# Kernel tuning notes

Hardware: AMD Instinct MI355X
Metric: run time of the kernel (lower is better)

## Reference

```python
import jax, jax.numpy as jnp
import numpy as np

N_NODES = 10000
IN_DIM = 256
HIDDEN = 512
OUT_DIM = 256
N_EDGES = 320000


def setup_inputs() -> dict:
    key = jax.random.key(0)
    k1, k2, k3, k4, k5, k6 = jax.random.split(key, 6)
    x = jax.random.normal(k1, (N_NODES, IN_DIM), dtype=jnp.float32)
    edge_index = jax.random.randint(k2, (2, N_EDGES), 0, N_NODES, dtype=jnp.int64)
    s1 = 1.0 / np.sqrt(2 * IN_DIM)
    s2 = 1.0 / np.sqrt(HIDDEN)
    W1 = jax.random.uniform(k3, (2 * IN_DIM, HIDDEN), jnp.float32, -s1, s1)
    b1 = jax.random.uniform(k4, (HIDDEN,), jnp.float32, -s1, s1)
    W2 = jax.random.uniform(k5, (HIDDEN, OUT_DIM), jnp.float32, -s2, s2)
    b2 = jax.random.uniform(k6, (OUT_DIM,), jnp.float32, -s2, s2)
    return {"x": x, "edge_index": edge_index, "W1": W1, "b1": b1, "W2": W2, "b2": b2}


def reference(x, edge_index, W1, b1, W2, b2):
    # x: [N, d]; edge_index: [2, E]
    x = x.reshape(-1, x.shape[-1])
    start, end = edge_index.reshape(2, -1)
    # gather + concat -> [E, 2d]
    ef = jnp.concatenate([x[start], x[end]], axis=1)
    h = jax.nn.relu(ef @ W1 + b1)          # [E, hidden]
    out = h @ W2 + b2                        # [E, out]
    return out.reshape(-1, edge_index.shape[1], out.shape[-1])  # [1, E, out]
```

## Files before the change

### kernel.cpp

```cpp
#include <hip/hip_runtime.h>
#include <cstdint>

#define E_TOTAL 320000
#define NN 10000
#define DIN 256
#define HDIM 512
#define DOUT 256
#define M_TILE 48
#define N_MAIN_BLOCKS ((E_TOTAL + M_TILE - 1) / M_TILE)

typedef __attribute__((ext_vector_type(8))) short short8;
typedef __attribute__((ext_vector_type(8))) unsigned short ushort8;
typedef __attribute__((ext_vector_type(4))) float f32x4;

__device__ __forceinline__ unsigned short f2bf(float f) {
    union { float f; unsigned u; } v; v.f = f;
    unsigned u = v.u;
    return (unsigned short)((u + 0x7fffu + ((u >> 16) & 1u)) >> 16);
}
__device__ __forceinline__ float bf2f(unsigned short u) {
    union { unsigned u; float f; } v; v.u = ((unsigned)u) << 16; return v.f;
}

__global__ void detect_i64(const int* __restrict__ eidx, int* __restrict__ flag) {
    __shared__ int anynz;
    if (threadIdx.x == 0) anynz = 0;
    __syncthreads();
    int v = 0;
    for (int i = threadIdx.x; i < 8192; i += blockDim.x) v |= eidx[2 * i + 1];
    if (v != 0) atomicOr(&anynz, 1);
    __syncthreads();
    if (threadIdx.x == 0) *flag = (anynz == 0) ? 1 : 0;
}

__global__ void convert_x(const float* __restrict__ x, unsigned short* __restrict__ xb) {
    int total = NN * DIN;
    for (int i = blockIdx.x * blockDim.x + threadIdx.x; i < total; i += gridDim.x * blockDim.x)
        xb[i] = f2bf(x[i]);
}

__global__ void pack_w(const float* __restrict__ W, unsigned short* __restrict__ Wp,
                       int ncols, int nct, int nks) {
    int tid = blockIdx.x * blockDim.x + threadIdx.x;
    int total = nct * nks * 64;
    if (tid >= total) return;
    int lane = tid & 63;
    int ks = (tid >> 6) % nks;
    int ct = tid / (64 * nks);
    int k0 = ks * 32 + (lane >> 4) * 8;
    int n = ct * 16 + (lane & 15);
    short8 v;
#pragma unroll
    for (int j = 0; j < 8; j++) v[j] = (short)f2bf(W[(long)(k0 + j) * ncols + n]);
    *(short8*)(Wp + ((long)(ct * nks + ks) * 64 + lane) * 8) = v;
}

__global__ void pack_wcat(const float* __restrict__ W1, unsigned short* __restrict__ Wp) {
    int tid = blockIdx.x * blockDim.x + threadIdx.x;
    if (tid >= 64 * 8 * 64) return;
    int lane = tid & 63;
    int ks = (tid >> 6) & 7;
    int ct = tid >> 9;
    int k0 = ks * 32 + (lane >> 4) * 8;
    int n = ct * 16 + (lane & 15);
    int col = n & 511;
    int radd = (n >> 9) * 256;
    short8 v;
#pragma unroll
    for (int j = 0; j < 8; j++) v[j] = (short)f2bf(W1[(long)(k0 + j + radd) * HDIM + col]);
    *(short8*)(Wp + ((long)(ct * 8 + ks) * 64 + lane) * 8) = v;
}

template<bool PF32>
__global__ __launch_bounds__(256, 2)
void node_gemm(const unsigned short* __restrict__ xb,
               const unsigned short* __restrict__ Wcp,
               void* __restrict__ Pv)
{
    __shared__ unsigned short xs[64 * 256];
    const int tid = threadIdx.x;
    const int lane = tid & 63;
    const int w = tid >> 6;
    const int lo = lane & 15;
    const int quad = lane >> 4;
    const int rt0 = blockIdx.x;
    const int cq = blockIdx.y;

#pragma unroll
    for (int i = 0; i < 8; i++) {
        int rp = i * 4 + w;
        int r = rp * 2 + (lane >> 5);
        int node = rt0 * 64 + r;
        if (node > NN - 1) node = NN - 1;
        int cs = (lane & 31) ^ (r & 7);
        const unsigned short* g = xb + (long)node * DIN + cs * 8;
        unsigned roff = __builtin_amdgcn_readfirstlane((unsigned)(rp * 512));
        __builtin_amdgcn_global_load_lds(
            (const __attribute__((address_space(1))) void*)g,
            (__attribute__((address_space(3))) void*)(xs + roff),
            16, 0, 0);
    }
    __syncthreads();

    f32x4 acc[4][4];
#pragma unroll
    for (int rt = 0; rt < 4; rt++)
#pragma unroll
        for (int ct = 0; ct < 4; ct++) acc[rt][ct] = (f32x4){0.f, 0.f, 0.f, 0.f};

    short8 ap[2][4], bp[2][4];
    auto loadA = [&](short8* d, int ks) {
#pragma unroll
        for (int rt = 0; rt < 4; rt++) {
            int m = rt * 16 + lo;
            int c = (ks * 4 + quad) ^ (m & 7);
            d[rt] = *(const short8*)(xs + m * 256 + c * 8);
        }
    };
    auto loadB = [&](short8* d, int ks) {
#pragma unroll
        for (int ct = 0; ct < 4; ct++) {
            int ctg = cq * 16 + w * 4 + ct;
            d[ct] = *(const short8*)(Wcp + ((long)(ctg * 8 + ks) * 64 + lane) * 8);
        }
    };
    loadA(ap[0], 0);
    loadB(bp[0], 0);
#pragma unroll
    for (int ks = 0; ks < 8; ks++) {
        int cur = ks & 1, nxt = cur ^ 1;
        if (ks < 7) { loadA(ap[nxt], ks + 1); loadB(bp[nxt], ks + 1); }
#pragma unroll
        for (int ct = 0; ct < 4; ct++)
#pragma unroll
            for (int rt = 0; rt < 4; rt++)
                acc[rt][ct] = __builtin_amdgcn_mfma_f32_16x16x32_bf16(
                    ap[cur][rt], bp[cur][ct], acc[rt][ct], 0, 0, 0);
    }

#pragma unroll
    for (int rt = 0; rt < 4; rt++) {
#pragma unroll
        for (int rr = 0; rr < 4; rr++) {
            int r = rt0 * 64 + rt * 16 + quad * 4 + rr;
            if (r < NN) {
                long off = (long)r * 1024 + cq * 256 + w * 64 + lo;
#pragma unroll
                for (int ct = 0; ct < 4; ct++) {
                    float v = acc[rt][ct][rr];
                    if constexpr (PF32) ((float*)Pv)[off + ct * 16] = v;
                    else ((unsigned short*)Pv)[off + ct * 16] = f2bf(v);
                }
            }
        }
    }
}

template<bool PF32>
__global__ __launch_bounds__(512, 4)
void edge_out(const void* __restrict__ Pv,
              const int* __restrict__ eidx,
              const float* __restrict__ b1,
              const unsigned short* __restrict__ W2p,
              const float* __restrict__ b2,
              const int* __restrict__ flag,
              float* __restrict__ out)
{
    __shared__ unsigned short hs[64 * 512];
    const int tid = threadIdx.x;
    const int lane = tid & 63;
    const int w = tid >> 6;
    const int lo = lane & 15;
    const int quad = lane >> 4;
    const long e0 = (long)blockIdx.x * 64;

    const bool is64 = (*flag != 0);
    int snv, tnv;
    {
        long e = e0 + w * 8 + (lane & 7);
        long s, t;
        if (is64) {
            s = ((const long long*)eidx)[e];
            t = ((const long long*)eidx)[E_TOTAL + e];
        } else {
            s = eidx[e];
            t = eidx[E_TOTAL + e];
        }
        if (s < 0) s = 0; if (s > NN - 1) s = NN - 1;
        if (t < 0) t = 0; if (t > NN - 1) t = NN - 1;
        snv = (int)s; tnv = (int)t;
    }
    f32x4 bia0 = *(const f32x4*)(b1 + lane * 8);
    f32x4 bia1 = *(const f32x4*)(b1 + lane * 8 + 4);

#pragma unroll
    for (int j = 0; j < 8; j++) {
        int sv = __shfl(snv, j, 8);
        int tv = __shfl(tnv, j, 8);
        int r = w * 8 + j;
        short8 hv;
        if constexpr (PF32) {
            const float* Ar = (const float*)Pv + (long)sv * 1024 + lane * 8;
            const float* Br = (const float*)Pv + (long)tv * 1024 + 512 + lane * 8;
            f32x4 a0 = *(const f32x4*)(Ar);
            f32x4 a1 = *(const f32x4*)(Ar + 4);
            f32x4 c0 = *(const f32x4*)(Br);
            f32x4 c1 = *(const f32x4*)(Br + 4);
#pragma unroll
            for (int jj = 0; jj < 4; jj++) {
                hv[jj]     = (short)f2bf(fmaxf(a0[jj] + c0[jj] + bia0[jj], 0.f));
                hv[jj + 4] = (short)f2bf(fmaxf(a1[jj] + c1[jj] + bia1[jj], 0.f));
            }
        } else {
            const unsigned short* Ar = (const unsigned short*)Pv + (long)sv * 1024 + lane * 8;
            const unsigned short* Br = (const unsigned short*)Pv + (long)tv * 1024 + 512 + lane * 8;
            ushort8 av = *(const ushort8*)(Ar);
            ushort8 cv = *(const ushort8*)(Br);
#pragma unroll
            for (int jj = 0; jj < 4; jj++) {
                hv[jj]     = (short)f2bf(fmaxf(bf2f(av[jj]) + bf2f(cv[jj]) + bia0[jj], 0.f));
                hv[jj + 4] = (short)f2bf(fmaxf(bf2f(av[jj + 4]) + bf2f(cv[jj + 4]) + bia1[jj], 0.f));
            }
        }
        *(short8*)(hs + r * 512 + ((lane ^ (r & 7)) << 3)) = hv;
    }
    __syncthreads();

    f32x4 oacc[4][2];
#pragma unroll
    for (int rt = 0; rt < 4; rt++)
#pragma unroll
        for (int ct = 0; ct < 2; ct++) oacc[rt][ct] = (f32x4){0.f, 0.f, 0.f, 0.f};

    short8 ap[2][4], bp[2][2];
    auto loadA2 = [&](short8* d, int ks) {
#pragma unroll
        for (int rt = 0; rt < 4; rt++) {
            int m = rt * 16 + lo;
            int c = (ks * 4 + quad) ^ (m & 7);
            d[rt] = *(const short8*)(hs + m * 512 + c * 8);
        }
    };
    auto loadB2 = [&](short8* d, int ks) {
#pragma unroll
        for (int ct = 0; ct < 2; ct++) {
            int ctg = w * 2 + ct;
            d[ct] = *(const short8*)(W2p + ((long)(ctg * 16 + ks) * 64 + lane) * 8);
        }
    };
    loadA2(ap[0], 0);
    loadB2(bp[0], 0);
#pragma unroll
    for (int ks = 0; ks < 16; ks++) {
        int cur = ks & 1, nxt = cur ^ 1;
        if (ks < 15) { loadA2(ap[nxt], ks + 1); loadB2(bp[nxt], ks + 1); }
#pragma unroll
        for (int ct = 0; ct < 2; ct++)
#pragma unroll
            for (int rt = 0; rt < 4; rt++)
                oacc[rt][ct] = __builtin_amdgcn_mfma_f32_16x16x32_bf16(
                    ap[cur][rt], bp[cur][ct], oacc[rt][ct], 0, 0, 0);
    }

    float bv[2];
#pragma unroll
    for (int ct = 0; ct < 2; ct++) bv[ct] = b2[w * 32 + ct * 16 + lo];
#pragma unroll
    for (int rt = 0; rt < 4; rt++) {
#pragma unroll
        for (int rr = 0; rr < 4; rr++) {
            int rwo = rt * 16 + quad * 4 + rr;
            float* op = out + (e0 + rwo) * DOUT + w * 32 + lo;
#pragma unroll
            for (int ct = 0; ct < 2; ct++)
                op[ct * 16] = oacc[rt][ct][rr] + bv[ct];
        }
    }
}

__global__ __launch_bounds__(256, 2)
void edge_mlp(const unsigned short* __restrict__ xb,
              const int* __restrict__ eidx,
              const float* __restrict__ b1,
              const unsigned short* __restrict__ W1p,
              const float* __restrict__ b2v_g,
              const unsigned short* __restrict__ W2p,
              const int* __restrict__ flag,
              float* __restrict__ out)
{
    __shared__ unsigned short ef[M_TILE * 512];
    __shared__ unsigned short hb[M_TILE * 128];

    const int tid = threadIdx.x;
    const int lane = tid & 63;
    const int w = tid >> 6;
    const int lo = lane & 15;
    const int quad = lane >> 4;
    const long e0 = (long)blockIdx.x * M_TILE;
    const bool is64 = (*flag != 0);

#pragma unroll
    for (int i = 0; i < 12; i++) {
        int r = i * 4 + w;
        long e = e0 + r;
        long ec = (e < E_TOTAL) ? e : 0;
        long sn, tn;
        if (is64) {
            sn = ((const long long*)eidx)[ec];
            tn = ((const long long*)eidx)[E_TOTAL + ec];
        } else {
            sn = eidx[ec];
            tn = eidx[E_TOTAL + ec];
        }
        long node = (lane < 32) ? sn : tn;
        int cih = (lane & 31) ^ (r & 7);
        const unsigned short* g = xb + node * DIN + cih * 8;
        unsigned roff = __builtin_amdgcn_readfirstlane((unsigned)(r * 512));
        __builtin_amdgcn_global_load_lds(
            (const __attribute__((address_space(1))) void*)g,
            (__attribute__((address_space(3))) void*)(ef + roff),
            16, 0, 0);
    }
    __syncthreads();

    f32x4 oacc[3][4];
#pragma unroll
    for (int rt = 0; rt < 3; rt++)
#pragma unroll
        for (int ct = 0; ct < 4; ct++)
            oacc[rt][ct] = (f32x4){0.f, 0.f, 0.f, 0.f};

    auto loadA1 = [&](short8* dst, int ks) {
#pragma unroll
        for (int rt = 0; rt < 3; rt++) {
            int m = rt * 16 + lo;
            int c = (ks * 4 + quad) ^ (m & 7);
            dst[rt] = *(const short8*)(ef + m * 512 + c * 8);
        }
    };

    for (int kc = 0; kc < 4; kc++) {
        short8 w2f[16];
#pragma unroll
        for (int s = 0; s < 4; s++)
#pragma unroll
            for (int ct = 0; ct < 4; ct++) {
                int ctg = w * 4 + ct;
                int ks2 = kc * 4 + s;
                w2f[s * 4 + ct] =
                    *(const short8*)(W2p + ((long)(ctg * 16 + ks2) * 64 + lane) * 8);
            }
        float b1v[2];
#pragma unroll
        for (int ct = 0; ct < 2; ct++) b1v[ct] = b1[kc * 128 + w * 32 + ct * 16 + lo];

        f32x4 hacc[3][2];
#pragma unroll
        for (int rt = 0; rt < 3; rt++)
#pragma unroll
            for (int ct = 0; ct < 2; ct++)
                hacc[rt][ct] = (f32x4){0.f, 0.f, 0.f, 0.f};

        short8 a_p[2][3], b_p[2][2];
        loadA1(a_p[0], 0);
#pragma unroll
        for (int ct = 0; ct < 2; ct++) {
            int ctg = kc * 8 + w * 2 + ct;
            b_p[0][ct] = *(const short8*)(W1p + ((long)(ctg * 16 + 0) * 64 + lane) * 8);
        }

#pragma unroll
        for (int ks = 0; ks < 16; ks++) {
            int cur = ks & 1, nxt = cur ^ 1;
            if (ks < 15) {
                loadA1(a_p[nxt], ks + 1);
#pragma unroll
                for (int ct = 0; ct < 2; ct++) {
                    int ctg = kc * 8 + w * 2 + ct;
                    b_p[nxt][ct] =
                        *(const short8*)(W1p + ((long)(ctg * 16 + ks + 1) * 64 + lane) * 8);
                }
            }
#pragma unroll
            for (int ct = 0; ct < 2; ct++)
#pragma unroll
                for (int rt = 0; rt < 3; rt++)
                    hacc[rt][ct] = __builtin_amdgcn_mfma_f32_16x16x32_bf16(
                        a_p[cur][rt], b_p[cur][ct], hacc[rt][ct], 0, 0, 0);
        }

#pragma unroll
        for (int ct = 0; ct < 2; ct++) {
            int cwl = w * 32 + ct * 16 + lo;
            float bias = b1v[ct];
            int c = cwl >> 3;
            int cb = cwl & 7;
#pragma unroll
            for (int rt = 0; rt < 3; rt++) {
#pragma unroll
                for (int rr = 0; rr < 4; rr++) {
                    int rw = rt * 16 + quad * 4 + rr;
                    float v = fmaxf(hacc[rt][ct][rr] + bias, 0.f);
                    hb[rw * 128 + ((c ^ (rw & 7)) << 3) + cb] = f2bf(v);
                }
            }
        }
        __syncthreads();

        short8 a2_p[2][3];
#pragma unroll
        for (int rt = 0; rt < 3; rt++) {
            int m = rt * 16 + lo;
            int c = (0 + quad) ^ (m & 7);
            a2_p[0][rt] = *(const short8*)(hb + m * 128 + c * 8);
        }
#pragma unroll
        for (int s = 0; s < 4; s++) {
            int cur = s & 1, nxt = cur ^ 1;
            if (s < 3) {
#pragma unroll
                for (int rt = 0; rt < 3; rt++) {
                    int m = rt * 16 + lo;
                    int c = ((s + 1) * 4 + quad) ^ (m & 7);
                    a2_p[nxt][rt] = *(const short8*)(hb + m * 128 + c * 8);
                }
            }
#pragma unroll
            for (int ct = 0; ct < 4; ct++)
#pragma unroll
                for (int rt = 0; rt < 3; rt++)
                    oacc[rt][ct] = __builtin_amdgcn_mfma_f32_16x16x32_bf16(
                        a2_p[cur][rt], w2f[s * 4 + ct], oacc[rt][ct], 0, 0, 0);
        }
        if (kc < 3) __syncthreads();
    }

    float bv[4];
#pragma unroll
    for (int ct = 0; ct < 4; ct++) bv[ct] = b2v_g[w * 64 + ct * 16 + lo];
#pragma unroll
    for (int rt = 0; rt < 3; rt++) {
#pragma unroll
        for (int rr = 0; rr < 4; rr++) {
            int rw = rt * 16 + quad * 4 + rr;
            long e = e0 + rw;
            if (e < E_TOTAL) {
                float* op = out + e * DOUT + w * 64 + lo;
#pragma unroll
                for (int ct = 0; ct < 4; ct++)
                    op[ct * 16] = oacc[rt][ct][rr] + bv[ct];
            }
        }
    }
}

extern "C" void kernel_launch(void* const* d_in, const int* in_sizes, int n_in,
                              void* d_out, int out_size, void* d_ws, size_t ws_size,
                              hipStream_t stream) {
    const float* x   = (const float*)d_in[0];
    const int*   ei  = (const int*)d_in[1];
    const float* W1  = (const float*)d_in[2];
    const float* b1  = (const float*)d_in[3];
    const float* W2  = (const float*)d_in[4];
    const float* b2  = (const float*)d_in[5];
    float* out = (float*)d_out;

    unsigned short* xb  = (unsigned short*)d_ws;
    unsigned short* Wcp = (unsigned short*)((char*)d_ws + 5120000);
    unsigned short* W2p = (unsigned short*)((char*)d_ws + 5644288);
    int* flag = (int*)((char*)d_ws + 5906432);
    void* P = (void*)((char*)d_ws + 5906496);
    const size_t NEED_F32  = 5906496ull + 40960000ull;
    const size_t NEED_BF16 = 5906496ull + 20480000ull;

    hipLaunchKernelGGL(detect_i64, dim3(1), dim3(256), 0, stream, ei, flag);
    hipLaunchKernelGGL(convert_x, dim3(1024), dim3(256), 0, stream, x, xb);
    hipLaunchKernelGGL(pack_w, dim3(64), dim3(256), 0, stream, W2, W2p, DOUT, 16, 16);

    if (ws_size >= NEED_F32) {
        hipLaunchKernelGGL(pack_wcat, dim3(128), dim3(256), 0, stream, W1, Wcp);
        hipLaunchKernelGGL((node_gemm<true>), dim3(157, 4), dim3(256), 0, stream, xb, Wcp, P);
        hipLaunchKernelGGL((edge_out<true>), dim3(5000), dim3(512), 0, stream,
                           P, ei, b1, W2p, b2, flag, out);
    } else if (ws_size >= NEED_BF16) {
        hipLaunchKernelGGL(pack_wcat, dim3(128), dim3(256), 0, stream, W1, Wcp);
        hipLaunchKernelGGL((node_gemm<false>), dim3(157, 4), dim3(256), 0, stream, xb, Wcp, P);
        hipLaunchKernelGGL((edge_out<false>), dim3(5000), dim3(512), 0, stream,
                           P, ei, b1, W2p, b2, flag, out);
    } else {
        hipLaunchKernelGGL(pack_w, dim3(128), dim3(256), 0, stream, W1, Wcp, HDIM, 32, 16);
        hipLaunchKernelGGL(edge_mlp, dim3(N_MAIN_BLOCKS), dim3(256), 0, stream,
                           xb, ei, b1, Wcp, b2, W2p, flag, out);
    }
}
```

Baseline: 565.1 us.

## Use bf16 node projections, batch gathers before compute, nontemporal output stores

The fp32 precomputed-node-projection path is dropped, so the bf16 intermediate P is always used when the workspace allows it. This halves gather traffic at the cost of extra rounding of the per-node partial products. The bf16 edge kernel now issues all 16 row gathers up front before doing the add/bias/relu and LDS writes, which raises memory-level parallelism at the cost of more registers. Output stores become nontemporal to avoid polluting cache with the large write-once result.

New measurement: 467.9 us. -17.2%, faster.

```diff
diff --git a/kernel.cpp b/kernel.cpp
--- a/kernel.cpp
+++ b/kernel.cpp
@@ -193,36 +193,50 @@
     f32x4 bia0 = *(const f32x4*)(b1 + lane * 8);
     f32x4 bia1 = *(const f32x4*)(b1 + lane * 8 + 4);
 
+    int svv[8], tvv[8];
 #pragma unroll
     for (int j = 0; j < 8; j++) {
-        int sv = __shfl(snv, j, 8);
-        int tv = __shfl(tnv, j, 8);
-        int r = w * 8 + j;
-        short8 hv;
-        if constexpr (PF32) {
-            const float* Ar = (const float*)Pv + (long)sv * 1024 + lane * 8;
-            const float* Br = (const float*)Pv + (long)tv * 1024 + 512 + lane * 8;
+        svv[j] = __shfl(snv, j, 8);
+        tvv[j] = __shfl(tnv, j, 8);
+    }
+
+    if constexpr (PF32) {
+#pragma unroll
+        for (int j = 0; j < 8; j++) {
+            int r = w * 8 + j;
+            const float* Ar = (const float*)Pv + (long)svv[j] * 1024 + lane * 8;
+            const float* Br = (const float*)Pv + (long)tvv[j] * 1024 + 512 + lane * 8;
             f32x4 a0 = *(const f32x4*)(Ar);
             f32x4 a1 = *(const f32x4*)(Ar + 4);
             f32x4 c0 = *(const f32x4*)(Br);
             f32x4 c1 = *(const f32x4*)(Br + 4);
+            short8 hv;
 #pragma unroll
             for (int jj = 0; jj < 4; jj++) {
                 hv[jj]     = (short)f2bf(fmaxf(a0[jj] + c0[jj] + bia0[jj], 0.f));
                 hv[jj + 4] = (short)f2bf(fmaxf(a1[jj] + c1[jj] + bia1[jj], 0.f));
             }
-        } else {
-            const unsigned short* Ar = (const unsigned short*)Pv + (long)sv * 1024 + lane * 8;
-            const unsigned short* Br = (const unsigned short*)Pv + (long)tv * 1024 + 512 + lane * 8;
-            ushort8 av = *(const ushort8*)(Ar);
-            ushort8 cv = *(const ushort8*)(Br);
+            *(short8*)(hs + r * 512 + ((lane ^ (r & 7)) << 3)) = hv;
+        }
+    } else {
+        const unsigned short* Pb = (const unsigned short*)Pv;
+        ushort8 pa[8], pt[8];
+#pragma unroll
+        for (int j = 0; j < 8; j++) {
+            pa[j] = *(const ushort8*)(Pb + (long)svv[j] * 1024 + lane * 8);
+            pt[j] = *(const ushort8*)(Pb + (long)tvv[j] * 1024 + 512 + lane * 8);
+        }
+#pragma unroll
+        for (int j = 0; j < 8; j++) {
+            int r = w * 8 + j;
+            short8 hv;
 #pragma unroll
             for (int jj = 0; jj < 4; jj++) {
-                hv[jj]     = (short)f2bf(fmaxf(bf2f(av[jj]) + bf2f(cv[jj]) + bia0[jj], 0.f));
-                hv[jj + 4] = (short)f2bf(fmaxf(bf2f(av[jj + 4]) + bf2f(cv[jj + 4]) + bia1[jj], 0.f));
-            }
-        }
-        *(short8*)(hs + r * 512 + ((lane ^ (r & 7)) << 3)) = hv;
+                hv[jj]     = (short)f2bf(fmaxf(bf2f(pa[j][jj]) + bf2f(pt[j][jj]) + bia0[jj], 0.f));
+                hv[jj + 4] = (short)f2bf(fmaxf(bf2f(pa[j][jj + 4]) + bf2f(pt[j][jj + 4]) + bia1[jj], 0.f));
+            }
+            *(short8*)(hs + r * 512 + ((lane ^ (r & 7)) << 3)) = hv;
+        }
     }
     __syncthreads();
 
@@ -273,7 +287,7 @@
             float* op = out + (e0 + rwo) * DOUT + w * 32 + lo;
 #pragma unroll
             for (int ct = 0; ct < 2; ct++)
-                op[ct * 16] = oacc[rt][ct][rr] + bv[ct];
+                __builtin_nontemporal_store(oacc[rt][ct][rr] + bv[ct], op + ct * 16);
         }
     }
 }
@@ -470,19 +484,13 @@
     unsigned short* W2p = (unsigned short*)((char*)d_ws + 5644288);
     int* flag = (int*)((char*)d_ws + 5906432);
     void* P = (void*)((char*)d_ws + 5906496);
-    const size_t NEED_F32  = 5906496ull + 40960000ull;
     const size_t NEED_BF16 = 5906496ull + 20480000ull;
 
     hipLaunchKernelGGL(detect_i64, dim3(1), dim3(256), 0, stream, ei, flag);
     hipLaunchKernelGGL(convert_x, dim3(1024), dim3(256), 0, stream, x, xb);
     hipLaunchKernelGGL(pack_w, dim3(64), dim3(256), 0, stream, W2, W2p, DOUT, 16, 16);
 
-    if (ws_size >= NEED_F32) {
-        hipLaunchKernelGGL(pack_wcat, dim3(128), dim3(256), 0, stream, W1, Wcp);
-        hipLaunchKernelGGL((node_gemm<true>), dim3(157, 4), dim3(256), 0, stream, xb, Wcp, P);
-        hipLaunchKernelGGL((edge_out<true>), dim3(5000), dim3(512), 0, stream,
-                           P, ei, b1, W2p, b2, flag, out);
-    } else if (ws_size >= NEED_BF16) {
+    if (ws_size >= NEED_BF16) {
         hipLaunchKernelGGL(pack_wcat, dim3(128), dim3(256), 0, stream, W1, Wcp);
         hipLaunchKernelGGL((node_gemm<false>), dim3(157, 4), dim3(256), 0, stream, xb, Wcp, P);
         hipLaunchKernelGGL((edge_out<false>), dim3(5000), dim3(512), 0, stream,
```
